# Kernel tuning notes

Measured on AMD Instinct MI355X. Metric: run time of the kernel, lower is better.

The kernel has to match this reference:

```python
import jax, jax.numpy as jnp
import numpy as np

B, S, HID = 2, 1024, 2048
HQ, HKV, HD = 32, 8, 64
ROPE_BASE = 10000.0

def _rope_tables(seq_len, head_dim):
    inv_freq = 1.0 / (ROPE_BASE ** (np.arange(0, head_dim, 2, dtype=np.float32) / head_dim))
    t = np.arange(seq_len, dtype=np.float32)
    freqs = np.outer(t, inv_freq)                      # [S, d/2]
    emb = np.concatenate([freqs, freqs], axis=-1)      # [S, d]
    return jnp.asarray(np.cos(emb)), jnp.asarray(np.sin(emb))

def setup_inputs() -> dict:
    key = jax.random.key(0)
    ks = jax.random.split(key, 5)
    cos, sin = _rope_tables(S, HD)
    return {
        'hidden_states': jax.random.normal(ks[0], (B, S, HID), jnp.float32),
        'cos': cos, 'sin': sin,
        'Wq': jax.random.normal(ks[1], (HID, HID), jnp.float32) * (HID ** -0.5),
        'Wk': jax.random.normal(ks[2], (HID, HKV * HD), jnp.float32) * (HID ** -0.5),
        'Wv': jax.random.normal(ks[3], (HID, HKV * HD), jnp.float32) * (HID ** -0.5),
        'Wo': jax.random.normal(ks[4], (HID, HID), jnp.float32) * (HID ** -0.5),
    }

def _rotate_half(x):
    d = x.shape[-1]
    return jnp.concatenate([-x[..., d // 2:], x[..., :d // 2]], axis=-1)

def reference(hidden_states, cos, sin, Wq, Wk, Wv, Wo):
    b, s, _ = hidden_states.shape
    q = (hidden_states @ Wq).reshape(b, s, HQ, HD)    # [b,s,Hq,d]
    k = (hidden_states @ Wk).reshape(b, s, HKV, HD)   # [b,s,Hkv,d]
    v = (hidden_states @ Wv).reshape(b, s, HKV, HD)
    # RoPE: cos/sin [s,d] broadcast as [s,1,d] over head dim
    c = cos[:, None, :]
    sn = sin[:, None, :]
    q = q * c + _rotate_half(q) * sn
    k = k * c + _rotate_half(k) * sn
    # GQA: expand kv heads to query heads (repeat_kv)
    n_rep = HQ // HKV
    k = jnp.repeat(k, n_rep, axis=2)                  # [b,s,Hq,d]
    v = jnp.repeat(v, n_rep, axis=2)
    scale = HD ** -0.5
    scores = jnp.einsum('bqhd,bkhd->bhqk', q, k) * scale  # [b,Hq,s,s]
    causal = jnp.tril(jnp.ones((s, s), bool))
    scores = jnp.where(causal, scores, jnp.float32(-1e30))
    probs = jax.nn.softmax(scores.astype(jnp.float32), axis=-1).astype(q.dtype)
    out = jnp.einsum('bhqk,bkhd->bqhd', probs, v).reshape(b, s, HID)
    return out @ Wo
```

## Files before the change

kernel.cpp:

```cpp
#include <hip/hip_runtime.h>
#include <math.h>

#define B_   2
#define S_   1024
#define HID_ 2048
#define HQ_  32
#define HKV_ 8
#define HD_  64
#define NQKV 3072

using short8  = __attribute__((ext_vector_type(8))) short;
using floatx4 = __attribute__((ext_vector_type(4))) float;

__device__ __forceinline__ unsigned short f2bf(float x) {
    unsigned int u = __builtin_bit_cast(unsigned int, x);
    u += 0x7FFFu + ((u >> 16) & 1u);
    return (unsigned short)(u >> 16);
}
__device__ __forceinline__ float bf2f(unsigned short u) {
    return __builtin_bit_cast(float, (unsigned int)u << 16);
}

__device__ __forceinline__ void gl_lds16(const unsigned short* g, unsigned short* l) {
    __builtin_amdgcn_global_load_lds(
        (const __attribute__((address_space(1))) void*)g,
        (__attribute__((address_space(3))) void*)l, 16, 0, 0);
}

template <bool BF16OUT>
__global__ __launch_bounds__(256) void gemm_mfma(const unsigned short* __restrict__ A,
                                                 const unsigned short* __restrict__ Bt,
                                                 void* __restrict__ Cv,
                                                 int M, int N, int K) {
    __shared__ __align__(16) unsigned short As[128 * 32];
    __shared__ __align__(16) unsigned short Bs[128 * 32];

    const int tid  = threadIdx.x;
    const int w    = tid >> 6;
    const int lane = tid & 63;
    const int col  = lane & 15;
    const int quad = lane >> 4;
    const int m0 = blockIdx.y * 128;
    const int n0 = blockIdx.x * 128;
    const int wm = (w >> 1) * 64;
    const int wn = (w & 1) * 64;

    const int srow = lane >> 2;
    const int skof = (lane & 3) * 8;
    const unsigned short* Ag = A  + (size_t)(m0 + srow) * K + skof;
    const unsigned short* Bg = Bt + (size_t)(n0 + srow) * K + skof;
    const int rb = w * 16;

    floatx4 acc[4][4] = {};

    for (int k0 = 0; k0 < K; k0 += 32) {
        gl_lds16(Ag + (size_t)(rb     ) * K + k0, &As[(rb     ) * 32]);
        gl_lds16(Ag + (size_t)(rb + 64) * K + k0, &As[(rb + 64) * 32]);
        gl_lds16(Bg + (size_t)(rb     ) * K + k0, &Bs[(rb     ) * 32]);
        gl_lds16(Bg + (size_t)(rb + 64) * K + k0, &Bs[(rb + 64) * 32]);
        __syncthreads();

        short8 af[4], bfr[4];
#pragma unroll
        for (int i = 0; i < 4; ++i)
            af[i] = *(const short8*)&As[(wm + i * 16 + col) * 32 + quad * 8];
#pragma unroll
        for (int j = 0; j < 4; ++j)
            bfr[j] = *(const short8*)&Bs[(wn + j * 16 + col) * 32 + quad * 8];
#pragma unroll
        for (int i = 0; i < 4; ++i)
#pragma unroll
            for (int j = 0; j < 4; ++j)
                acc[i][j] = __builtin_amdgcn_mfma_f32_16x16x32_bf16(
                    af[i], bfr[j], acc[i][j], 0, 0, 0);
        __syncthreads();
    }

#pragma unroll
    for (int i = 0; i < 4; ++i)
#pragma unroll
        for (int j = 0; j < 4; ++j)
#pragma unroll
            for (int r = 0; r < 4; ++r) {
                size_t off = (size_t)(m0 + wm + i * 16 + quad * 4 + r) * N
                           + (n0 + wn + j * 16 + col);
                if constexpr (BF16OUT)
                    ((unsigned short*)Cv)[off] = f2bf(acc[i][j][r]);
                else
                    ((float*)Cv)[off] = acc[i][j][r];
            }
}

__global__ __launch_bounds__(256) void convert_x(const float* __restrict__ in,
                                                 unsigned short* __restrict__ out) {
    int tid = blockIdx.x * 256 + threadIdx.x;
    float4 v = *(const float4*)&in[(size_t)tid * 4];
    ushort4 o = {f2bf(v.x), f2bf(v.y), f2bf(v.z), f2bf(v.w)};
    *(ushort4*)&out[(size_t)tid * 4] = o;
}

__global__ __launch_bounds__(256) void transpose_all(const float* __restrict__ Wq,
                                                     const float* __restrict__ Wk,
                                                     const float* __restrict__ Wv,
                                                     const float* __restrict__ Wo,
                                                     unsigned short* __restrict__ WcatT,
                                                     unsigned short* __restrict__ WoT) {
    __shared__ float tile[32][33];
    int bid = blockIdx.x;
    const float* W;
    unsigned short* WT;
    int N, tn0, tk0;
    if (bid < 4096) {
        W = Wq; WT = WcatT; N = HID_;
        tn0 = (bid & 63) * 32; tk0 = (bid >> 6) * 32;
    } else if (bid < 5120) {
        bid -= 4096;
        W = Wk; WT = WcatT + (size_t)HID_ * HID_; N = 512;
        tn0 = (bid & 15) * 32; tk0 = (bid >> 4) * 32;
    } else if (bid < 6144) {
        bid -= 5120;
        W = Wv; WT = WcatT + (size_t)(HID_ + 512) * HID_; N = 512;
        tn0 = (bid & 15) * 32; tk0 = (bid >> 4) * 32;
    } else {
        bid -= 6144;
        W = Wo; WT = WoT; N = HID_;
        tn0 = (bid & 63) * 32; tk0 = (bid >> 6) * 32;
    }
    const int r  = threadIdx.x >> 3;
    const int c4 = (threadIdx.x & 7) * 4;
    float4 v = *(const float4*)&W[(size_t)(tk0 + r) * N + tn0 + c4];
    tile[r][c4 + 0] = v.x;
    tile[r][c4 + 1] = v.y;
    tile[r][c4 + 2] = v.z;
    tile[r][c4 + 3] = v.w;
    __syncthreads();
    ushort4 o = {f2bf(tile[c4 + 0][r]), f2bf(tile[c4 + 1][r]),
                 f2bf(tile[c4 + 2][r]), f2bf(tile[c4 + 3][r])};
    *(ushort4*)&WT[(size_t)(tn0 + r) * HID_ + tk0 + c4] = o;
}

__global__ __launch_bounds__(256) void convert_qkv(const unsigned short* __restrict__ QKV,
                                                   const float* __restrict__ cosT,
                                                   const float* __restrict__ sinT,
                                                   unsigned short* __restrict__ Qbf,
                                                   unsigned short* __restrict__ Kbf,
                                                   unsigned short* __restrict__ Vt) {
    int tid = blockIdx.x * 256 + threadIdx.x;
    const int NQ = B_ * S_ * HQ_ * 32;
    const int NK = B_ * S_ * HKV_ * 32;
    if (tid < NQ) {
        int d = tid & 31;
        int h = (tid >> 5) & (HQ_ - 1);
        int s = (tid >> 10) & (S_ - 1);
        int b = tid >> 20;
        const unsigned short* row = QKV + (size_t)(b * S_ + s) * NQKV + h * HD_;
        float x0 = bf2f(row[d]), x1 = bf2f(row[d + 32]);
        float c0 = cosT[s * HD_ + d],      s0 = sinT[s * HD_ + d];
        float c1 = cosT[s * HD_ + d + 32], s1 = sinT[s * HD_ + d + 32];
        unsigned short* orow = Qbf + ((size_t)(b * HQ_ + h) * S_ + s) * HD_;
        orow[d]      = f2bf((x0 * c0 - x1 * s0) * 0.125f);
        orow[d + 32] = f2bf((x1 * c1 + x0 * s1) * 0.125f);
    } else if (tid < NQ + NK) {
        tid -= NQ;
        int d  = tid & 31;
        int kv = (tid >> 5) & (HKV_ - 1);
        int s  = (tid >> 8) & (S_ - 1);
        int b  = tid >> 18;
        const unsigned short* row = QKV + (size_t)(b * S_ + s) * NQKV + HID_ + kv * HD_;
        float x0 = bf2f(row[d]), x1 = bf2f(row[d + 32]);
        float c0 = cosT[s * HD_ + d],      s0 = sinT[s * HD_ + d];
        float c1 = cosT[s * HD_ + d + 32], s1 = sinT[s * HD_ + d + 32];
        unsigned short* orow = Kbf + ((size_t)(b * HKV_ + kv) * S_ + s) * HD_;
        orow[d]      = f2bf(x0 * c0 - x1 * s0);
        orow[d + 32] = f2bf(x1 * c1 + x0 * s1);
    } else {
        tid -= NQ + NK;
        int s4 = tid & 255;
        int d  = (tid >> 8) & (HD_ - 1);
        int kv = (tid >> 14) & (HKV_ - 1);
        int b  = tid >> 17;
        int s  = s4 * 4;
        const unsigned short* base =
            QKV + (size_t)b * S_ * NQKV + HID_ + 512 + kv * HD_ + d;
        ushort4 o;
        o.x = base[(size_t)(s + 0) * NQKV];
        o.y = base[(size_t)(s + 1) * NQKV];
        o.z = base[(size_t)(s + 2) * NQKV];
        o.w = base[(size_t)(s + 3) * NQKV];
        *(ushort4*)&Vt[((size_t)(b * HKV_ + kv) * HD_ + d) * S_ + s] = o;
    }
}

__global__ __launch_bounds__(256) void attn_mfma(const unsigned short* __restrict__ Qbf,
                                                 const unsigned short* __restrict__ Kbf,
                                                 const unsigned short* __restrict__ Vt,
                                                 unsigned short* __restrict__ Ctx) {
    const int t  = 63 - blockIdx.x;
    const int kv = blockIdx.y;
    const int b  = blockIdx.z;
    const int w    = threadIdx.x >> 6;
    const int lane = threadIdx.x & 63;
    const int col  = lane & 15;
    const int quad = lane >> 4;

    const int h   = kv * 4 + w;
    const int bh  = b * HQ_ + h;
    const int bkv = b * HKV_ + kv;
    const int qw  = 16 * t;
    const int myq = qw + col;

    __shared__ __align__(16) unsigned short sK[2][64 * 32];
    __shared__ __align__(16) unsigned short sV[2][64 * 32];
    __shared__ __align__(16) unsigned short sP[4][16 * 72];
    unsigned short* myP = sP[w];

    const unsigned short* qrow = Qbf + ((size_t)bh * S_ + qw + col) * HD_;
    short8 bq0 = *(const short8*)&qrow[quad * 8];
    short8 bq1 = *(const short8*)&qrow[32 + quad * 8];

    const unsigned short* Kbase = Kbf + (size_t)bkv * S_ * HD_;
    const unsigned short* Vbase = Vt  + (size_t)bkv * HD_ * S_;

    const int srow = 16 * w + (lane >> 2);
    const int sch  = (lane & 3) * 8;
    unsigned short* dK0 = &sK[0][16 * w * 32];
    unsigned short* dK1 = &sK[1][16 * w * 32];
    unsigned short* dV0 = &sV[0][16 * w * 32];
    unsigned short* dV1 = &sV[1][16 * w * 32];

    floatx4 acc[4] = {};
    float m_i = -1e30f, l_i = 0.f;
    const int nsteps = (16 * t + 79) >> 6;

    for (int it = 0; it < nsteps; ++it) {
        const int k0 = it * 64;
        gl_lds16(Kbase + (size_t)(k0 + srow) * HD_ + sch,      dK0);
        gl_lds16(Kbase + (size_t)(k0 + srow) * HD_ + 32 + sch, dK1);
        gl_lds16(Vbase + (size_t)srow * S_ + k0 + sch,         dV0);
        gl_lds16(Vbase + (size_t)srow * S_ + k0 + 32 + sch,    dV1);
        __syncthreads();

        floatx4 sc[4];
#pragma unroll
        for (int tt = 0; tt < 4; ++tt) {
            short8 ak0 = *(const short8*)&sK[0][(16 * tt + col) * 32 + quad * 8];
            short8 ak1 = *(const short8*)&sK[1][(16 * tt + col) * 32 + quad * 8];
            floatx4 z = {0.f, 0.f, 0.f, 0.f};
            z = __builtin_amdgcn_mfma_f32_16x16x32_bf16(ak0, bq0, z, 0, 0, 0);
            z = __builtin_amdgcn_mfma_f32_16x16x32_bf16(ak1, bq1, z, 0, 0, 0);
            sc[tt] = z;
        }
        if (k0 + 63 > qw) {
#pragma unroll
            for (int tt = 0; tt < 4; ++tt)
#pragma unroll
                for (int r = 0; r < 4; ++r)
                    if (k0 + 16 * tt + quad * 4 + r > myq) sc[tt][r] = -1e30f;
        }
        float vmax = sc[0][0];
#pragma unroll
        for (int tt = 0; tt < 4; ++tt)
#pragma unroll
            for (int r = 0; r < 4; ++r)
                vmax = fmaxf(vmax, sc[tt][r]);
        vmax = fmaxf(vmax, __shfl_xor(vmax, 16, 64));
        vmax = fmaxf(vmax, __shfl_xor(vmax, 32, 64));
        const float mnew  = fmaxf(m_i, vmax);
        const float alpha = __expf(m_i - mnew);
        m_i = mnew;
        float lsum = 0.f;
#pragma unroll
        for (int tt = 0; tt < 4; ++tt) {
            float p0 = __expf(sc[tt][0] - mnew);
            float p1 = __expf(sc[tt][1] - mnew);
            float p2 = __expf(sc[tt][2] - mnew);
            float p3 = __expf(sc[tt][3] - mnew);
            lsum += (p0 + p1) + (p2 + p3);
            ushort4 pk = {f2bf(p0), f2bf(p1), f2bf(p2), f2bf(p3)};
            *(ushort4*)&myP[col * 72 + 16 * tt + quad * 4] = pk;
        }
        lsum += __shfl_xor(lsum, 16, 64);
        lsum += __shfl_xor(lsum, 32, 64);
        l_i = l_i * alpha + lsum;
        float a_r[4];
#pragma unroll
        for (int r = 0; r < 4; ++r)
            a_r[r] = __shfl(alpha, quad * 4 + r, 64);
#pragma unroll
        for (int nt = 0; nt < 4; ++nt)
#pragma unroll
            for (int r = 0; r < 4; ++r)
                acc[nt][r] *= a_r[r];
        short8 pa0 = *(const short8*)&myP[col * 72 + quad * 8];
        short8 pa1 = *(const short8*)&myP[col * 72 + 32 + quad * 8];
#pragma unroll
        for (int nt = 0; nt < 4; ++nt) {
            short8 vb0 = *(const short8*)&sV[0][(nt * 16 + col) * 32 + quad * 8];
            short8 vb1 = *(const short8*)&sV[1][(nt * 16 + col) * 32 + quad * 8];
            acc[nt] = __builtin_amdgcn_mfma_f32_16x16x32_bf16(pa0, vb0, acc[nt], 0, 0, 0);
            acc[nt] = __builtin_amdgcn_mfma_f32_16x16x32_bf16(pa1, vb1, acc[nt], 0, 0, 0);
        }
        __syncthreads();
    }

    const float invl = 1.0f / l_i;
    float inv_r[4];
#pragma unroll
    for (int r = 0; r < 4; ++r)
        inv_r[r] = __shfl(invl, quad * 4 + r, 64);
#pragma unroll
    for (int nt = 0; nt < 4; ++nt)
#pragma unroll
        for (int r = 0; r < 4; ++r)
            Ctx[(size_t)(b * S_ + qw + quad * 4 + r) * HID_ + h * HD_ + nt * 16 + col] =
                f2bf(acc[nt][r] * inv_r[r]);
}

extern "C" void kernel_launch(void* const* d_in, const int* in_sizes, int n_in,
                              void* d_out, int out_size, void* d_ws, size_t ws_size,
                              hipStream_t stream) {
    const float* X    = (const float*)d_in[0];
    const float* cosT = (const float*)d_in[1];
    const float* sinT = (const float*)d_in[2];
    const float* Wq   = (const float*)d_in[3];
    const float* Wk   = (const float*)d_in[4];
    const float* Wv   = (const float*)d_in[5];
    const float* Wo   = (const float*)d_in[6];

    const int M = B_ * S_;
    const size_t MB = 1024u * 1024u;

    char* ws = (char*)d_ws;
    unsigned short* Xbf   = (unsigned short*)(ws);
    unsigned short* Qbf   = (unsigned short*)(ws);
    unsigned short* WcatT = (unsigned short*)(ws + 8 * MB);
    unsigned short* Kbf   = (unsigned short*)(ws + 8 * MB);
    unsigned short* Vt    = (unsigned short*)(ws + 10 * MB);
    unsigned short* Ctxbf = (unsigned short*)(ws + 12 * MB);
    unsigned short* WoT   = (unsigned short*)(ws + 20 * MB);
    unsigned short* QKVbf = (unsigned short*)d_out;
    float* out = (float*)d_out;

    convert_x<<<(M * HID_ / 4) / 256, 256, 0, stream>>>(X, Xbf);

    transpose_all<<<10240, 256, 0, stream>>>(Wq, Wk, Wv, Wo, WcatT, WoT);

    gemm_mfma<true><<<dim3(NQKV / 128, M / 128), 256, 0, stream>>>(
        Xbf, WcatT, QKVbf, M, NQKV, HID_);

    {
        int total = B_ * S_ * HQ_ * 32 + B_ * S_ * HKV_ * 32
                  + B_ * HKV_ * HD_ * (S_ / 4);
        convert_qkv<<<total / 256, 256, 0, stream>>>(QKVbf, cosT, sinT, Qbf, Kbf, Vt);
    }

    attn_mfma<<<dim3(64, HKV_, B_), 256, 0, stream>>>(Qbf, Kbf, Vt, Ctxbf);

    gemm_mfma<false><<<dim3(HID_ / 128, M / 128), 256, 0, stream>>>(
        Ctxbf, WoT, out, M, HID_, HID_);
}
```

Before: 263.0 us.

## Fuse RoPE into QKV GEMM epilogue, merge prep kernels, retile GEMMs to 64x128

New measurement: 264.1 us. No clear change (+0.4%).

```diff
diff --git a/kernel.cpp b/kernel.cpp
--- a/kernel.cpp
+++ b/kernel.cpp
@@ -7,7 +7,6 @@
 #define HQ_  32
 #define HKV_ 8
 #define HD_  64
-#define NQKV 3072
 
 using short8  = __attribute__((ext_vector_type(8))) short;
 using floatx4 = __attribute__((ext_vector_type(4))) float;
@@ -27,102 +26,42 @@
         (__attribute__((address_space(3))) void*)l, 16, 0, 0);
 }
 
-template <bool BF16OUT>
-__global__ __launch_bounds__(256) void gemm_mfma(const unsigned short* __restrict__ A,
-                                                 const unsigned short* __restrict__ Bt,
-                                                 void* __restrict__ Cv,
-                                                 int M, int N, int K) {
-    __shared__ __align__(16) unsigned short As[128 * 32];
-    __shared__ __align__(16) unsigned short Bs[128 * 32];
-
-    const int tid  = threadIdx.x;
-    const int w    = tid >> 6;
-    const int lane = tid & 63;
-    const int col  = lane & 15;
-    const int quad = lane >> 4;
-    const int m0 = blockIdx.y * 128;
-    const int n0 = blockIdx.x * 128;
-    const int wm = (w >> 1) * 64;
-    const int wn = (w & 1) * 64;
-
-    const int srow = lane >> 2;
-    const int skof = (lane & 3) * 8;
-    const unsigned short* Ag = A  + (size_t)(m0 + srow) * K + skof;
-    const unsigned short* Bg = Bt + (size_t)(n0 + srow) * K + skof;
-    const int rb = w * 16;
-
-    floatx4 acc[4][4] = {};
-
-    for (int k0 = 0; k0 < K; k0 += 32) {
-        gl_lds16(Ag + (size_t)(rb     ) * K + k0, &As[(rb     ) * 32]);
-        gl_lds16(Ag + (size_t)(rb + 64) * K + k0, &As[(rb + 64) * 32]);
-        gl_lds16(Bg + (size_t)(rb     ) * K + k0, &Bs[(rb     ) * 32]);
-        gl_lds16(Bg + (size_t)(rb + 64) * K + k0, &Bs[(rb + 64) * 32]);
-        __syncthreads();
-
-        short8 af[4], bfr[4];
-#pragma unroll
-        for (int i = 0; i < 4; ++i)
-            af[i] = *(const short8*)&As[(wm + i * 16 + col) * 32 + quad * 8];
-#pragma unroll
-        for (int j = 0; j < 4; ++j)
-            bfr[j] = *(const short8*)&Bs[(wn + j * 16 + col) * 32 + quad * 8];
-#pragma unroll
-        for (int i = 0; i < 4; ++i)
-#pragma unroll
-            for (int j = 0; j < 4; ++j)
-                acc[i][j] = __builtin_amdgcn_mfma_f32_16x16x32_bf16(
-                    af[i], bfr[j], acc[i][j], 0, 0, 0);
-        __syncthreads();
-    }
-
-#pragma unroll
-    for (int i = 0; i < 4; ++i)
-#pragma unroll
-        for (int j = 0; j < 4; ++j)
-#pragma unroll
-            for (int r = 0; r < 4; ++r) {
-                size_t off = (size_t)(m0 + wm + i * 16 + quad * 4 + r) * N
-                           + (n0 + wn + j * 16 + col);
-                if constexpr (BF16OUT)
-                    ((unsigned short*)Cv)[off] = f2bf(acc[i][j][r]);
-                else
-                    ((float*)Cv)[off] = acc[i][j][r];
-            }
-}
-
-__global__ __launch_bounds__(256) void convert_x(const float* __restrict__ in,
-                                                 unsigned short* __restrict__ out) {
-    int tid = blockIdx.x * 256 + threadIdx.x;
-    float4 v = *(const float4*)&in[(size_t)tid * 4];
-    ushort4 o = {f2bf(v.x), f2bf(v.y), f2bf(v.z), f2bf(v.w)};
-    *(ushort4*)&out[(size_t)tid * 4] = o;
-}
-
-__global__ __launch_bounds__(256) void transpose_all(const float* __restrict__ Wq,
-                                                     const float* __restrict__ Wk,
-                                                     const float* __restrict__ Wv,
-                                                     const float* __restrict__ Wo,
-                                                     unsigned short* __restrict__ WcatT,
-                                                     unsigned short* __restrict__ WoT) {
+__global__ __launch_bounds__(256) void prep_all(const float* __restrict__ X,
+                                                const float* __restrict__ Wq,
+                                                const float* __restrict__ Wk,
+                                                const float* __restrict__ Wv,
+                                                const float* __restrict__ Wo,
+                                                unsigned short* __restrict__ Xbf,
+                                                unsigned short* __restrict__ WcatT,
+                                                unsigned short* __restrict__ WoT) {
     __shared__ float tile[32][33];
     int bid = blockIdx.x;
+    if (bid < 4096) {
+        int tid = bid * 256 + threadIdx.x;
+        float4 v = *(const float4*)&X[(size_t)tid * 4];
+        ushort4 o = {f2bf(v.x), f2bf(v.y), f2bf(v.z), f2bf(v.w)};
+        *(ushort4*)&Xbf[(size_t)tid * 4] = o;
+        return;
+    }
     const float* W;
     unsigned short* WT;
     int N, tn0, tk0;
-    if (bid < 4096) {
-        W = Wq; WT = WcatT; N = HID_;
-        tn0 = (bid & 63) * 32; tk0 = (bid >> 6) * 32;
-    } else if (bid < 5120) {
+    if (bid < 10240) {
         bid -= 4096;
-        W = Wk; WT = WcatT + (size_t)HID_ * HID_; N = 512;
-        tn0 = (bid & 15) * 32; tk0 = (bid >> 4) * 32;
-    } else if (bid < 6144) {
-        bid -= 5120;
-        W = Wv; WT = WcatT + (size_t)(HID_ + 512) * HID_; N = 512;
-        tn0 = (bid & 15) * 32; tk0 = (bid >> 4) * 32;
+        if (bid < 4096) {
+            W = Wq; WT = WcatT; N = HID_;
+            tn0 = (bid & 63) * 32; tk0 = (bid >> 6) * 32;
+        } else if (bid < 5120) {
+            bid -= 4096;
+            W = Wk; WT = WcatT + (size_t)HID_ * HID_; N = 512;
+            tn0 = (bid & 15) * 32; tk0 = (bid >> 4) * 32;
+        } else {
+            bid -= 5120;
+            W = Wv; WT = WcatT + (size_t)(HID_ + 512) * HID_; N = 512;
+            tn0 = (bid & 15) * 32; tk0 = (bid >> 4) * 32;
+        }
     } else {
-        bid -= 6144;
+        bid -= 10240;
         W = Wo; WT = WoT; N = HID_;
         tn0 = (bid & 63) * 32; tk0 = (bid >> 6) * 32;
     }
@@ -139,63 +78,136 @@
     *(ushort4*)&WT[(size_t)(tn0 + r) * HID_ + tk0 + c4] = o;
 }
 
-__global__ __launch_bounds__(256) void convert_qkv(const unsigned short* __restrict__ QKV,
-                                                   const float* __restrict__ cosT,
-                                                   const float* __restrict__ sinT,
-                                                   unsigned short* __restrict__ Qbf,
-                                                   unsigned short* __restrict__ Kbf,
-                                                   unsigned short* __restrict__ Vt) {
-    int tid = blockIdx.x * 256 + threadIdx.x;
-    const int NQ = B_ * S_ * HQ_ * 32;
-    const int NK = B_ * S_ * HKV_ * 32;
-    if (tid < NQ) {
-        int d = tid & 31;
-        int h = (tid >> 5) & (HQ_ - 1);
-        int s = (tid >> 10) & (S_ - 1);
-        int b = tid >> 20;
-        const unsigned short* row = QKV + (size_t)(b * S_ + s) * NQKV + h * HD_;
-        float x0 = bf2f(row[d]), x1 = bf2f(row[d + 32]);
-        float c0 = cosT[s * HD_ + d],      s0 = sinT[s * HD_ + d];
-        float c1 = cosT[s * HD_ + d + 32], s1 = sinT[s * HD_ + d + 32];
-        unsigned short* orow = Qbf + ((size_t)(b * HQ_ + h) * S_ + s) * HD_;
-        orow[d]      = f2bf((x0 * c0 - x1 * s0) * 0.125f);
-        orow[d + 32] = f2bf((x1 * c1 + x0 * s1) * 0.125f);
-    } else if (tid < NQ + NK) {
-        tid -= NQ;
-        int d  = tid & 31;
-        int kv = (tid >> 5) & (HKV_ - 1);
-        int s  = (tid >> 8) & (S_ - 1);
-        int b  = tid >> 18;
-        const unsigned short* row = QKV + (size_t)(b * S_ + s) * NQKV + HID_ + kv * HD_;
-        float x0 = bf2f(row[d]), x1 = bf2f(row[d + 32]);
-        float c0 = cosT[s * HD_ + d],      s0 = sinT[s * HD_ + d];
-        float c1 = cosT[s * HD_ + d + 32], s1 = sinT[s * HD_ + d + 32];
-        unsigned short* orow = Kbf + ((size_t)(b * HKV_ + kv) * S_ + s) * HD_;
-        orow[d]      = f2bf(x0 * c0 - x1 * s0);
-        orow[d + 32] = f2bf(x1 * c1 + x0 * s1);
+__global__ __launch_bounds__(256) void gemm_qkv(const unsigned short* __restrict__ A,
+                                                const unsigned short* __restrict__ Bt,
+                                                const float* __restrict__ cosT,
+                                                const float* __restrict__ sinT,
+                                                unsigned short* __restrict__ Qbf,
+                                                unsigned short* __restrict__ Kbf,
+                                                unsigned short* __restrict__ Vnat) {
+    __shared__ __align__(16) unsigned short As[64 * 32];
+    __shared__ __align__(16) unsigned short Bs[128 * 32];
+
+    const int m0 = (blockIdx.x / 24) * 64;
+    const int n0 = (blockIdx.x % 24) * 128;
+
+    const int tid  = threadIdx.x;
+    const int w    = tid >> 6;
+    const int lane = tid & 63;
+    const int col  = lane & 15;
+    const int quad = lane >> 4;
+    const int wm = (w >> 1) * 32;
+    const int wn = (w & 1) * 64;
+
+    const int lane16 = lane & 15;
+    const int lchunk = lane >> 4;
+    const unsigned short* Ag  = A  + (size_t)(m0 + 16 * w + lane16) * HID_ + lchunk * 8;
+    const unsigned short* Bg0 = Bt + (size_t)(n0 + 16 * w + lane16) * HID_ + lchunk * 8;
+    const unsigned short* Bg1 = Bt + (size_t)(n0 + 64 + 16 * w + lane16) * HID_ + lchunk * 8;
+
+    floatx4 acc[2][4] = {};
+
+    for (int k0 = 0; k0 < HID_; k0 += 32) {
+        gl_lds16(Ag  + k0, &As[w * 512]);
+        gl_lds16(Bg0 + k0, &Bs[w * 512]);
+        gl_lds16(Bg1 + k0, &Bs[(4 + w) * 512]);
+        __syncthreads();
+
+        short8 af[2], bfr[4];
+#pragma unroll
+        for (int i = 0; i < 2; ++i)
+            af[i] = *(const short8*)&As[((w >> 1) * 2 + i) * 512 + quad * 128 + col * 8];
+#pragma unroll
+        for (int j = 0; j < 4; ++j)
+            bfr[j] = *(const short8*)&Bs[((w & 1) * 4 + j) * 512 + quad * 128 + col * 8];
+#pragma unroll
+        for (int i = 0; i < 2; ++i)
+#pragma unroll
+            for (int j = 0; j < 4; ++j)
+                acc[i][j] = __builtin_amdgcn_mfma_f32_16x16x32_bf16(
+                    af[i], bfr[j], acc[i][j], 0, 0, 0);
+        __syncthreads();
+    }
+
+    if (n0 < 2048) {
+        const int h = (n0 + wn) >> 6;
+#pragma unroll
+        for (int i = 0; i < 2; ++i)
+#pragma unroll
+            for (int r = 0; r < 4; ++r) {
+                int srow = m0 + wm + i * 16 + quad * 4 + r;
+                int b = srow >> 10, s = srow & 1023;
+                unsigned short* base = Qbf + ((size_t)(b * HQ_ + h) * S_ + s) * HD_;
+#pragma unroll
+                for (int j = 0; j < 2; ++j) {
+                    int d = j * 16 + col;
+                    float x0 = acc[i][j][r], x1 = acc[i][j + 2][r];
+                    float c0 = cosT[s * HD_ + d],      s0c = sinT[s * HD_ + d];
+                    float c1 = cosT[s * HD_ + d + 32], s1c = sinT[s * HD_ + d + 32];
+                    base[d]      = f2bf((x0 * c0 - x1 * s0c) * 0.125f);
+                    base[d + 32] = f2bf((x1 * c1 + x0 * s1c) * 0.125f);
+                }
+            }
+    } else if (n0 < 2560) {
+        const int kvh = (n0 - 2048 + wn) >> 6;
+#pragma unroll
+        for (int i = 0; i < 2; ++i)
+#pragma unroll
+            for (int r = 0; r < 4; ++r) {
+                int srow = m0 + wm + i * 16 + quad * 4 + r;
+                int b = srow >> 10, s = srow & 1023;
+                unsigned short* base = Kbf + ((size_t)(b * HKV_ + kvh) * S_ + s) * HD_;
+#pragma unroll
+                for (int j = 0; j < 2; ++j) {
+                    int d = j * 16 + col;
+                    float x0 = acc[i][j][r], x1 = acc[i][j + 2][r];
+                    float c0 = cosT[s * HD_ + d],      s0c = sinT[s * HD_ + d];
+                    float c1 = cosT[s * HD_ + d + 32], s1c = sinT[s * HD_ + d + 32];
+                    base[d]      = f2bf(x0 * c0 - x1 * s0c);
+                    base[d + 32] = f2bf(x1 * c1 + x0 * s1c);
+                }
+            }
     } else {
-        tid -= NQ + NK;
-        int s4 = tid & 255;
-        int d  = (tid >> 8) & (HD_ - 1);
-        int kv = (tid >> 14) & (HKV_ - 1);
-        int b  = tid >> 17;
-        int s  = s4 * 4;
-        const unsigned short* base =
-            QKV + (size_t)b * S_ * NQKV + HID_ + 512 + kv * HD_ + d;
-        ushort4 o;
-        o.x = base[(size_t)(s + 0) * NQKV];
-        o.y = base[(size_t)(s + 1) * NQKV];
-        o.z = base[(size_t)(s + 2) * NQKV];
-        o.w = base[(size_t)(s + 3) * NQKV];
-        *(ushort4*)&Vt[((size_t)(b * HKV_ + kv) * HD_ + d) * S_ + s] = o;
-    }
+        const int kvh = (n0 - 2560 + wn) >> 6;
+#pragma unroll
+        for (int i = 0; i < 2; ++i)
+#pragma unroll
+            for (int r = 0; r < 4; ++r) {
+                int srow = m0 + wm + i * 16 + quad * 4 + r;
+                int b = srow >> 10, s = srow & 1023;
+                unsigned short* base = Vnat + ((size_t)(b * HKV_ + kvh) * S_ + s) * HD_;
+#pragma unroll
+                for (int j = 0; j < 4; ++j)
+                    base[j * 16 + col] = f2bf(acc[i][j][r]);
+            }
+    }
+}
+
+__global__ __launch_bounds__(256) void convert_vt(const unsigned short* __restrict__ Vnat,
+                                                  unsigned short* __restrict__ Vt) {
+    __shared__ unsigned short tile[64][72];
+    const int bkv = blockIdx.x >> 4;
+    const int s0  = (blockIdx.x & 15) * 64;
+    const int tid = threadIdx.x;
+    const int row = tid >> 2;
+    const int dp  = (tid & 3) * 16;
+
+    const unsigned short* src = Vnat + ((size_t)bkv * S_ + s0 + row) * HD_ + dp;
+#pragma unroll
+    for (int j = 0; j < 16; ++j)
+        tile[dp + j][row] = src[j];
+    __syncthreads();
+
+    unsigned short* dst = Vt + ((size_t)bkv * HD_ + row) * S_ + s0 + dp;
+    *(short8*)&dst[0] = *(const short8*)&tile[row][dp];
+    *(short8*)&dst[8] = *(const short8*)&tile[row][dp + 8];
 }
 
 __global__ __launch_bounds__(256) void attn_mfma(const unsigned short* __restrict__ Qbf,
                                                  const unsigned short* __restrict__ Kbf,
                                                  const unsigned short* __restrict__ Vt,
                                                  unsigned short* __restrict__ Ctx) {
-    const int t  = 63 - blockIdx.x;
+    const int t = 63 - ((blockIdx.x + 4 * (blockIdx.y + 8 * blockIdx.z)) & 63);
     const int kv = blockIdx.y;
     const int b  = blockIdx.z;
     const int w    = threadIdx.x >> 6;
@@ -209,8 +221,10 @@
     const int qw  = 16 * t;
     const int myq = qw + col;
 
-    __shared__ __align__(16) unsigned short sK[2][64 * 32];
-    __shared__ __align__(16) unsigned short sV[2][64 * 32];
+    __shared__ __align__(16) unsigned short sK0[64 * 32];
+    __shared__ __align__(16) unsigned short sK1[64 * 32];
+    __shared__ __align__(16) unsigned short sV0[64 * 32];
+    __shared__ __align__(16) unsigned short sV1[64 * 32];
     __shared__ __align__(16) unsigned short sP[4][16 * 72];
     unsigned short* myP = sP[w];
 
@@ -218,15 +232,12 @@
     short8 bq0 = *(const short8*)&qrow[quad * 8];
     short8 bq1 = *(const short8*)&qrow[32 + quad * 8];
 
-    const unsigned short* Kbase = Kbf + (size_t)bkv * S_ * HD_;
-    const unsigned short* Vbase = Vt  + (size_t)bkv * HD_ * S_;
-
-    const int srow = 16 * w + (lane >> 2);
-    const int sch  = (lane & 3) * 8;
-    unsigned short* dK0 = &sK[0][16 * w * 32];
-    unsigned short* dK1 = &sK[1][16 * w * 32];
-    unsigned short* dV0 = &sV[0][16 * w * 32];
-    unsigned short* dV1 = &sV[1][16 * w * 32];
+    const int lane16 = lane & 15;
+    const int lchunk = lane >> 4;
+    const unsigned short* KbL =
+        Kbf + (size_t)bkv * S_ * HD_ + (size_t)(16 * w + lane16) * HD_ + lchunk * 8;
+    const unsigned short* VbL =
+        Vt + (size_t)bkv * HD_ * S_ + (size_t)(16 * w + lane16) * S_ + lchunk * 8;
 
     floatx4 acc[4] = {};
     float m_i = -1e30f, l_i = 0.f;
@@ -234,17 +245,17 @@
 
     for (int it = 0; it < nsteps; ++it) {
         const int k0 = it * 64;
-        gl_lds16(Kbase + (size_t)(k0 + srow) * HD_ + sch,      dK0);
-        gl_lds16(Kbase + (size_t)(k0 + srow) * HD_ + 32 + sch, dK1);
-        gl_lds16(Vbase + (size_t)srow * S_ + k0 + sch,         dV0);
-        gl_lds16(Vbase + (size_t)srow * S_ + k0 + 32 + sch,    dV1);
+        gl_lds16(KbL + (size_t)k0 * HD_,      &sK0[w * 512]);
+        gl_lds16(KbL + (size_t)k0 * HD_ + 32, &sK1[w * 512]);
+        gl_lds16(VbL + k0,                    &sV0[w * 512]);
+        gl_lds16(VbL + k0 + 32,               &sV1[w * 512]);
         __syncthreads();
 
         floatx4 sc[4];
 #pragma unroll
         for (int tt = 0; tt < 4; ++tt) {
-            short8 ak0 = *(const short8*)&sK[0][(16 * tt + col) * 32 + quad * 8];
-            short8 ak1 = *(const short8*)&sK[1][(16 * tt + col) * 32 + quad * 8];
+            short8 ak0 = *(const short8*)&sK0[tt * 512 + quad * 128 + col * 8];
+            short8 ak1 = *(const short8*)&sK1[tt * 512 + quad * 128 + col * 8];
             floatx4 z = {0.f, 0.f, 0.f, 0.f};
             z = __builtin_amdgcn_mfma_f32_16x16x32_bf16(ak0, bq0, z, 0, 0, 0);
             z = __builtin_amdgcn_mfma_f32_16x16x32_bf16(ak1, bq1, z, 0, 0, 0);
@@ -295,8 +306,8 @@
         short8 pa1 = *(const short8*)&myP[col * 72 + 32 + quad * 8];
 #pragma unroll
         for (int nt = 0; nt < 4; ++nt) {
-            short8 vb0 = *(const short8*)&sV[0][(nt * 16 + col) * 32 + quad * 8];
-            short8 vb1 = *(const short8*)&sV[1][(nt * 16 + col) * 32 + quad * 8];
+            short8 vb0 = *(const short8*)&sV0[nt * 512 + quad * 128 + col * 8];
+            short8 vb1 = *(const short8*)&sV1[nt * 512 + quad * 128 + col * 8];
             acc[nt] = __builtin_amdgcn_mfma_f32_16x16x32_bf16(pa0, vb0, acc[nt], 0, 0, 0);
             acc[nt] = __builtin_amdgcn_mfma_f32_16x16x32_bf16(pa1, vb1, acc[nt], 0, 0, 0);
         }
@@ -314,6 +325,63 @@
         for (int r = 0; r < 4; ++r)
             Ctx[(size_t)(b * S_ + qw + quad * 4 + r) * HID_ + h * HD_ + nt * 16 + col] =
                 f2bf(acc[nt][r] * inv_r[r]);
+}
+
+__global__ __launch_bounds__(256) void gemm_wo(const unsigned short* __restrict__ A,
+                                               const unsigned short* __restrict__ Bt,
+                                               float* __restrict__ C) {
+    __shared__ __align__(16) unsigned short As[64 * 32];
+    __shared__ __align__(16) unsigned short Bs[128 * 32];
+
+    const int m0 = (blockIdx.x >> 4) * 64;
+    const int n0 = (blockIdx.x & 15) * 128;
+
+    const int tid  = threadIdx.x;
+    const int w    = tid >> 6;
+    const int lane = tid & 63;
+    const int col  = lane & 15;
+    const int quad = lane >> 4;
+    const int wm = (w >> 1) * 32;
+    const int wn = (w & 1) * 64;
+
+    const int lane16 = lane & 15;
+    const int lchunk = lane >> 4;
+    const unsigned short* Ag  = A  + (size_t)(m0 + 16 * w + lane16) * HID_ + lchunk * 8;
+    const unsigned short* Bg0 = Bt + (size_t)(n0 + 16 * w + lane16) * HID_ + lchunk * 8;
+    const unsigned short* Bg1 = Bt + (size_t)(n0 + 64 + 16 * w + lane16) * HID_ + lchunk * 8;
+
+    floatx4 acc[2][4] = {};
+
+    for (int k0 = 0; k0 < HID_; k0 += 32) {
+        gl_lds16(Ag  + k0, &As[w * 512]);
+        gl_lds16(Bg0 + k0, &Bs[w * 512]);
+        gl_lds16(Bg1 + k0, &Bs[(4 + w) * 512]);
+        __syncthreads();
+
+        short8 af[2], bfr[4];
+#pragma unroll
+        for (int i = 0; i < 2; ++i)
+            af[i] = *(const short8*)&As[((w >> 1) * 2 + i) * 512 + quad * 128 + col * 8];
+#pragma unroll
+        for (int j = 0; j < 4; ++j)
+            bfr[j] = *(const short8*)&Bs[((w & 1) * 4 + j) * 512 + quad * 128 + col * 8];
+#pragma unroll
+        for (int i = 0; i < 2; ++i)
+#pragma unroll
+            for (int j = 0; j < 4; ++j)
+                acc[i][j] = __builtin_amdgcn_mfma_f32_16x16x32_bf16(
+                    af[i], bfr[j], acc[i][j], 0, 0, 0);
+        __syncthreads();
+    }
+
+#pragma unroll
+    for (int i = 0; i < 2; ++i)
+#pragma unroll
+        for (int j = 0; j < 4; ++j)
+#pragma unroll
+            for (int r = 0; r < 4; ++r)
+                C[(size_t)(m0 + wm + i * 16 + quad * 4 + r) * HID_
+                  + (n0 + wn + j * 16 + col)] = acc[i][j][r];
 }
 
 extern "C" void kernel_launch(void* const* d_in, const int* in_sizes, int n_in,
@@ -327,35 +395,26 @@
     const float* Wv   = (const float*)d_in[5];
     const float* Wo   = (const float*)d_in[6];
 
-    const int M = B_ * S_;
     const size_t MB = 1024u * 1024u;
 
     char* ws = (char*)d_ws;
     unsigned short* Xbf   = (unsigned short*)(ws);
-    unsigned short* Qbf   = (unsigned short*)(ws);
+    unsigned short* Ctxbf = (unsigned short*)(ws);
     unsigned short* WcatT = (unsigned short*)(ws + 8 * MB);
-    unsigned short* Kbf   = (unsigned short*)(ws + 8 * MB);
-    unsigned short* Vt    = (unsigned short*)(ws + 10 * MB);
-    unsigned short* Ctxbf = (unsigned short*)(ws + 12 * MB);
     unsigned short* WoT   = (unsigned short*)(ws + 20 * MB);
-    unsigned short* QKVbf = (unsigned short*)d_out;
+    unsigned short* Qbf   = (unsigned short*)d_out;
+    unsigned short* Kbf   = (unsigned short*)((char*)d_out + 8 * MB);
+    unsigned short* Vnat  = (unsigned short*)((char*)d_out + 10 * MB);
+    unsigned short* Vt    = (unsigned short*)((char*)d_out + 12 * MB);
     float* out = (float*)d_out;
 
-    convert_x<<<(M * HID_ / 4) / 256, 256, 0, stream>>>(X, Xbf);
-
-    transpose_all<<<10240, 256, 0, stream>>>(Wq, Wk, Wv, Wo, WcatT, WoT);
-
-    gemm_mfma<true><<<dim3(NQKV / 128, M / 128), 256, 0, stream>>>(
-        Xbf, WcatT, QKVbf, M, NQKV, HID_);
-
-    {
-        int total = B_ * S_ * HQ_ * 32 + B_ * S_ * HKV_ * 32
-                  + B_ * HKV_ * HD_ * (S_ / 4);
-        convert_qkv<<<total / 256, 256, 0, stream>>>(QKVbf, cosT, sinT, Qbf, Kbf, Vt);
-    }
+    prep_all<<<14336, 256, 0, stream>>>(X, Wq, Wk, Wv, Wo, Xbf, WcatT, WoT);
+
+    gemm_qkv<<<768, 256, 0, stream>>>(Xbf, WcatT, cosT, sinT, Qbf, Kbf, Vnat);
+
+    convert_vt<<<256, 256, 0, stream>>>(Vnat, Vt);
 
     attn_mfma<<<dim3(64, HKV_, B_), 256, 0, stream>>>(Qbf, Kbf, Vt, Ctxbf);
 
-    gemm_mfma<false><<<dim3(HID_ / 128, M / 128), 256, 0, stream>>>(
-        Ctxbf, WoT, out, M, HID_, HID_);
-}
+    gemm_wo<<<512, 256, 0, stream>>>(Ctxbf, WoT, out);
+}
```
